# Kernel tuning notes

Hardware: AMD Instinct MI355X
Metric: run time of the kernel (lower is better)

The kernel has to match this reference:

```python
import jax, jax.numpy as jnp
import numpy as np

LN_EPS = 1e-5

def _layer_norm(x):
    m = jnp.mean(x, axis=-1, keepdims=True)
    v = jnp.mean(jnp.square(x - m), axis=-1, keepdims=True)
    return (x - m) / jnp.sqrt(v + LN_EPS)

def setup_inputs() -> dict:
    key = jax.random.key(0)
    ks = jax.random.split(key, 6)
    B, S, d_in, d_out = 8, 2048, 1024, 4096
    x = jax.random.normal(ks[0], (B, S, d_in), dtype=jnp.float32)
    # torch.randn % 1 -> values in [0, 1)
    weight_in = jax.random.uniform(ks[1], (d_out, d_in), dtype=jnp.float32)
    bias_in = jax.random.uniform(ks[2], (d_out,), dtype=jnp.float32)
    weight_out = jax.random.uniform(ks[3], (d_in, d_out), dtype=jnp.float32)
    bias_out = jax.random.uniform(ks[4], (d_in,), dtype=jnp.float32)
    lengths = jax.random.randint(ks[5], (B,), 1, S + 1, dtype=jnp.int64 if jax.config.read('jax_enable_x64') else jnp.int32)
    return {"x": x, "weight_in": weight_in, "bias_in": bias_in,
            "weight_out": weight_out, "bias_out": bias_out, "lengths": lengths}

def reference(x, weight_in, bias_in, weight_out, bias_out, lengths):
    # lengths is unused mathematically in the dense baseline (ragged kernels
    # only skip padded rows; valid-region math identical).
    for _ in range(10):
        x = jnp.einsum('bsd,od->bso', x, weight_in) + bias_in  # [B,S,d_out]
        x = _layer_norm(x)
        x = jnp.einsum('bso,do->bsd', x, weight_out) + bias_out  # [B,S,d_in]
        x = _layer_norm(x)
    return x
```

## Files before the change

kernel.cpp:

```cpp
#include <hip/hip_runtime.h>


typedef __attribute__((ext_vector_type(4))) float    f32x4;
typedef __attribute__((ext_vector_type(8))) _Float16 f16x8;
typedef __attribute__((ext_vector_type(4))) _Float16 f16x4;
typedef __attribute__((ext_vector_type(4))) uint     u32x4;

#define LN_EPS 1e-5f

__device__ __forceinline__ ushort f2h_bits(float f) {
    union { _Float16 h; ushort u; } c; c.h = (_Float16)f; return c.u;
}

typedef const __attribute__((address_space(1))) void* gas_ptr;
typedef __attribute__((address_space(3))) void* las_ptr;

__device__ __forceinline__ void gload_lds16(const void* g, void* l) {
    __builtin_amdgcn_global_load_lds((gas_ptr)g, (las_ptr)l, 16, 0, 0);
}

__device__ __forceinline__ f16x8 ldf(const _Float16* base, int byteoff) {
    return *reinterpret_cast<const f16x8*>(
        reinterpret_cast<const char*>(base) + byteoff);
}

__global__ __launch_bounds__(256) void conv_f32_f16(
        const float* __restrict__ in, _Float16* __restrict__ outp, int n4) {
    int i = blockIdx.x * 256 + threadIdx.x;
    if (i >= n4) return;
    float4 f = reinterpret_cast<const float4*>(in)[i];
    f16x4 r;
    r[0] = (_Float16)f.x; r[1] = (_Float16)f.y;
    r[2] = (_Float16)f.z; r[3] = (_Float16)f.w;
    *reinterpret_cast<f16x4*>(&outp[(size_t)i * 4]) = r;
}

template<int W>
__global__ __launch_bounds__(256)
void rowsum_rows(const _Float16* __restrict__ w, float* __restrict__ outp) {
    const int wid  = threadIdx.x >> 6;
    const int lane = threadIdx.x & 63;
    const size_t row = (size_t)blockIdx.x * 4 + wid;
    const _Float16* p = w + row * W;
    float s = 0.f;
    #pragma unroll
    for (int i = 0; i < W / 512; ++i) {
        f16x8 v = *reinterpret_cast<const f16x8*>(p + i * 512 + lane * 8);
        #pragma unroll
        for (int j = 0; j < 8; ++j) s += (float)v[j];
    }
    #pragma unroll
    for (int off = 32; off > 0; off >>= 1) s += __shfl_xor(s, off);
    if (lane == 0) outp[row] = s;
}

template<int M, int N, int K, bool FIRST>
__global__ __launch_bounds__(512)
void gemm256_ln(const _Float16* __restrict__ A, const _Float16* __restrict__ B,
                const float* __restrict__ bias, const float* __restrict__ wsum,
                const float2* __restrict__ pin, _Float16* __restrict__ C,
                float2* __restrict__ partials) {
    constexpr int NT   = K / 64;
    constexpr int NIT  = NT / 2;
    constexpr int NBX  = N / 256;
    constexpr int NWG  = (M / 256) * NBX;
    constexpr int NPIN = K / 256;

    __shared__ __attribute__((aligned(16))) _Float16 lds[2][2][2][8192];

    const int tid  = threadIdx.x;
    const int wid  = tid >> 6;
    const int lane = tid & 63;
    const int wr   = wid >> 2;
    const int wc   = wid & 3;

    int bn0, bm0;
    if constexpr (NBX == 16) {
        const int x = blockIdx.x & 7, j = blockIdx.x >> 3;
        bn0 = (x * 2 + (j & 1)) * 256;
        bm0 = (j >> 1) * 256;
    } else {
        int bid = (blockIdx.x & 7) * (NWG >> 3) + (blockIdx.x >> 3);
        bn0 = (bid % NBX) * 256;
        bm0 = (bid / NBX) * 256;
    }

    const int trow = tid >> 3;
    const int cg   = (tid & 7) ^ (trow & 7);
    const _Float16* Asrc = A + (size_t)(bm0 + trow) * K + cg * 8;
    const _Float16* Bsrc = B + (size_t)(bn0 + trow) * K + cg * 8;

    const int fr  = lane & 15;
    const int fq  = lane >> 4;
    const int s8  = lane & 7;
    const int cb0 = ((fq       ^ s8) << 4);
    const int cb1 = (((4 + fq) ^ s8) << 4);
    const int brb = (wc & 1) * 64;

    const _Float16* Ah[2] = { &lds[0][0][wr][0],      &lds[1][0][wr][0] };
    const _Float16* Bh[2] = { &lds[0][1][wc >> 1][0], &lds[1][1][wc >> 1][0] };

    f32x4 acc[8][4] = {};
    f16x8 aLo[4][2], aHi[4][2], bLo[2][2], bHi[2][2];

#define STAGE_A(buf, h, kk) do { \
    gload_lds16(Asrc + (size_t)((h)*128     ) * K + (kk), (void*)&lds[buf][0][h][       wid*512]); \
    gload_lds16(Asrc + (size_t)((h)*128 + 64) * K + (kk), (void*)&lds[buf][0][h][4096 + wid*512]); } while(0)
#define STAGE_B(buf, h, kk) do { \
    gload_lds16(Bsrc + (size_t)((h)*128     ) * K + (kk), (void*)&lds[buf][1][h][       wid*512]); \
    gload_lds16(Bsrc + (size_t)((h)*128 + 64) * K + (kk), (void*)&lds[buf][1][h][4096 + wid*512]); } while(0)

#define READ_ALO(b) do { _Pragma("unroll") for (int i = 0; i < 4; ++i) { \
    aLo[i][0] = ldf(Ah[b], (i*16+fr)*128 + cb0); \
    aLo[i][1] = ldf(Ah[b], (i*16+fr)*128 + cb1); } } while(0)
#define READ_AHI(b) do { _Pragma("unroll") for (int i = 0; i < 4; ++i) { \
    aHi[i][0] = ldf(Ah[b], ((i+4)*16+fr)*128 + cb0); \
    aHi[i][1] = ldf(Ah[b], ((i+4)*16+fr)*128 + cb1); } } while(0)
#define READ_BLO(b) do { _Pragma("unroll") for (int j = 0; j < 2; ++j) { \
    bLo[j][0] = ldf(Bh[b], (brb + j*16 + fr)*128 + cb0); \
    bLo[j][1] = ldf(Bh[b], (brb + j*16 + fr)*128 + cb1); } } while(0)
#define READ_BHI(b) do { _Pragma("unroll") for (int j = 0; j < 2; ++j) { \
    bHi[j][0] = ldf(Bh[b], (brb + (j+2)*16 + fr)*128 + cb0); \
    bHi[j][1] = ldf(Bh[b], (brb + (j+2)*16 + fr)*128 + cb1); } } while(0)

#define MFMA_BLK(AF, ioff, BF, joff) do { \
    _Pragma("unroll") for (int i = 0; i < 4; ++i) \
    _Pragma("unroll") for (int j = 0; j < 2; ++j) { \
        acc[i+ioff][j+joff] = __builtin_amdgcn_mfma_f32_16x16x32_f16(AF[i][0], BF[j][0], acc[i+ioff][j+joff], 0, 0, 0); \
        acc[i+ioff][j+joff] = __builtin_amdgcn_mfma_f32_16x16x32_f16(AF[i][1], BF[j][1], acc[i+ioff][j+joff], 0, 0, 0); } } while(0)

#define BARRIER() __builtin_amdgcn_s_barrier()
#define VMCNT4()  asm volatile("s_waitcnt vmcnt(4)" ::: "memory")
#define VMCNT0()  asm volatile("s_waitcnt vmcnt(0)" ::: "memory")

    STAGE_B(0, 0, 0);  STAGE_B(0, 1, 0);
    STAGE_A(0, 0, 0);  STAGE_A(0, 1, 0);
    STAGE_B(1, 0, 64); STAGE_B(1, 1, 64);

    float st_mean = 0.f, st_rstd = 1.f;
    if constexpr (!FIRST) {
        const int row  = tid >> 1;
        const int half = tid & 1;
        const float2* pr = pin + (size_t)(bm0 + row) * NPIN + half * (NPIN / 2);
        float s = 0.f, q = 0.f;
        #pragma unroll
        for (int k = 0; k < NPIN / 2; ++k) { s += pr[k].x; q += pr[k].y; }
        s += __shfl_xor(s, 1); q += __shfl_xor(q, 1);
        st_mean = s * (1.0f / K);
        const float var = fmaxf(q * (1.0f / K) - st_mean * st_mean, 0.f);
        st_rstd = rsqrtf(var + LN_EPS);
    }

    VMCNT4();
    BARRIER();

    float bcol[4], wcol[4];
    #pragma unroll
    for (int j = 0; j < 4; ++j) {
        const int c = bn0 + wc * 64 + j * 16 + fr;
        bcol[j] = bias[c]; wcol[j] = wsum[c];
    }

    for (int it = 0; it < NIT; ++it) {
        const int k1 = it * 128 + 64;
        const int k2 = (it * 128 + 128) & (K - 1);
        const int k3 = (it * 128 + 192) & (K - 1);
        const bool pf = (it < NIT - 1);

        READ_ALO(0); READ_BLO(0);
        STAGE_A(1, 0, k1);
        BARRIER();
        __builtin_amdgcn_s_setprio(1); MFMA_BLK(aLo, 0, bLo, 0); __builtin_amdgcn_s_setprio(0);
        BARRIER();
        READ_BHI(0);
        STAGE_A(1, 1, k1);
        BARRIER();
        __builtin_amdgcn_s_setprio(1); MFMA_BLK(aLo, 0, bHi, 2); __builtin_amdgcn_s_setprio(0);
        BARRIER();
        READ_AHI(0);
        if (pf) STAGE_B(0, 0, k2);
        BARRIER();
        __builtin_amdgcn_s_setprio(1); MFMA_BLK(aHi, 4, bLo, 0); __builtin_amdgcn_s_setprio(0);
        BARRIER();
        if (pf) STAGE_B(0, 1, k2);
        BARRIER();
        __builtin_amdgcn_s_setprio(1); MFMA_BLK(aHi, 4, bHi, 2); __builtin_amdgcn_s_setprio(0);
        if (pf) VMCNT4(); else VMCNT0();
        BARRIER();
        READ_ALO(1); READ_BLO(1);
        if (pf) STAGE_A(0, 0, k2);
        BARRIER();
        __builtin_amdgcn_s_setprio(1); MFMA_BLK(aLo, 0, bLo, 0); __builtin_amdgcn_s_setprio(0);
        BARRIER();
        READ_BHI(1);
        if (pf) STAGE_A(0, 1, k2);
        BARRIER();
        __builtin_amdgcn_s_setprio(1); MFMA_BLK(aLo, 0, bHi, 2); __builtin_amdgcn_s_setprio(0);
        BARRIER();
        READ_AHI(1);
        if (pf) STAGE_B(1, 0, k3);
        BARRIER();
        __builtin_amdgcn_s_setprio(1); MFMA_BLK(aHi, 4, bLo, 0); __builtin_amdgcn_s_setprio(0);
        BARRIER();
        if (pf) STAGE_B(1, 1, k3);
        BARRIER();
        __builtin_amdgcn_s_setprio(1); MFMA_BLK(aHi, 4, bHi, 2); __builtin_amdgcn_s_setprio(0);
        VMCNT4();
        BARRIER();
    }

    float2* sst = (float2*)&lds[0][0][0][0];
    if ((tid & 1) == 0) sst[tid >> 1] = make_float2(st_mean, st_rstd);
    __syncthreads();

    ushort* eps = (ushort*)&lds[1][0][0][0];
    #pragma unroll
    for (int pass = 0; pass < 4; ++pass) {
        if (wr == (pass >> 1)) {
            #pragma unroll
            for (int i2 = 0; i2 < 4; ++i2) {
                const int i = (pass & 1) * 4 + i2;
                #pragma unroll
                for (int q = 0; q < 4; ++q) {
                    const int rloc = wr * 128 + i * 16 + fq * 4 + q;
                    const int rl   = rloc - pass * 64;
                    const float2 st = sst[rloc];
                    const float rs = st.y, coef = st.y * st.x;
                    const int key = ((rl >> 2) & 3) << 4;
                    #pragma unroll
                    for (int j = 0; j < 4; ++j) {
                        const float v = rs * acc[i][j][q] - coef * wcol[j] + bcol[j];
                        const int c = wc * 64 + j * 16 + fr;
                        eps[rl * 256 + (c ^ key)] = f2h_bits(v);
                    }
                }
            }
        }
        BARRIER();
        {
            const int rl  = tid >> 3;
            const int a8  = tid & 7;
            const int r   = bm0 + pass * 64 + rl;
            const int key = ((rl >> 2) & 3) << 4;
            float s = 0.f, sq = 0.f;
            ushort* crow = (ushort*)(C + (size_t)r * N + bn0);
            #pragma unroll
            for (int k = 0; k < 4; ++k) {
                const int ch = 8 * k + a8;
                u32x4 d = *reinterpret_cast<const u32x4*>(&eps[rl * 256 + ch * 8]);
                const f16x8 v = *reinterpret_cast<const f16x8*>(&d);
                #pragma unroll
                for (int e = 0; e < 8; ++e) {
                    const float f = (float)v[e];
                    s += f; sq += f * f;
                }
                *reinterpret_cast<u32x4*>(&crow[(ch * 8) ^ key]) = d;
            }
            s  += __shfl_xor(s, 1);  sq += __shfl_xor(sq, 1);
            s  += __shfl_xor(s, 2);  sq += __shfl_xor(sq, 2);
            s  += __shfl_xor(s, 4);  sq += __shfl_xor(sq, 4);
            if (a8 == 0)
                partials[(size_t)r * NBX + (bn0 >> 8)] = make_float2(s, sq);
        }
        BARRIER();
    }
#undef STAGE_A
#undef STAGE_B
#undef READ_ALO
#undef READ_AHI
#undef READ_BLO
#undef READ_BHI
#undef MFMA_BLK
#undef BARRIER
#undef VMCNT4
#undef VMCNT0
}

__global__ __launch_bounds__(256)
void ln_final(const _Float16* __restrict__ a, const float2* __restrict__ part,
              float* __restrict__ outp) {
    const int wid  = threadIdx.x >> 6;
    const int lane = threadIdx.x & 63;
    const size_t row = (size_t)blockIdx.x * 4 + wid;

    float s = 0.f, q = 0.f;
    if (lane < 4) { const float2 p = part[row * 4 + lane]; s = p.x; q = p.y; }
    s += __shfl_xor(s, 1); q += __shfl_xor(q, 1);
    s += __shfl_xor(s, 2); q += __shfl_xor(q, 2);
    s = __shfl(s, 0); q = __shfl(q, 0);
    const float mean = s * (1.0f / 1024.f);
    const float var  = fmaxf(q * (1.0f / 1024.f) - mean * mean, 0.f);
    const float rstd = rsqrtf(var + LN_EPS);

    const _Float16* p = a + row * 1024;
    #pragma unroll
    for (int i = 0; i < 2; ++i) {
        f16x8 v = *reinterpret_cast<const f16x8*>(p + i * 512 + lane * 8);
        float* op = outp + row * 1024 + i * 512 + lane * 8;
        float4 o0, o1;
        o0.x = ((float)v[0] - mean) * rstd;
        o0.y = ((float)v[1] - mean) * rstd;
        o0.z = ((float)v[2] - mean) * rstd;
        o0.w = ((float)v[3] - mean) * rstd;
        o1.x = ((float)v[4] - mean) * rstd;
        o1.y = ((float)v[5] - mean) * rstd;
        o1.z = ((float)v[6] - mean) * rstd;
        o1.w = ((float)v[7] - mean) * rstd;
        reinterpret_cast<float4*>(op)[0] = o0;
        reinterpret_cast<float4*>(op)[1] = o1;
    }
}

extern "C" void kernel_launch(void* const* d_in, const int* in_sizes, int n_in,
                              void* d_out, int out_size, void* d_ws, size_t ws_size,
                              hipStream_t stream) {
    const float* x     = (const float*)d_in[0];
    const float* w_in  = (const float*)d_in[1];
    const float* b_in  = (const float*)d_in[2];
    const float* w_out = (const float*)d_in[3];
    const float* b_out = (const float*)d_in[4];

    constexpr int Mrows = 16384;
    constexpr int Din   = 1024;
    constexpr int Dout  = 4096;

    char* ws = (char*)d_ws;
    _Float16* wib = (_Float16*)ws; ws += (size_t)Dout * Din * 2;
    _Float16* wob = (_Float16*)ws; ws += (size_t)Din * Dout * 2;
    _Float16* a2b = (_Float16*)ws; ws += (size_t)Mrows * Din * 2;
    _Float16* a1b = (_Float16*)ws; ws += (size_t)Mrows * Dout * 2;
    float* winsum  = (float*)ws;   ws += Dout * 4;
    float* woutsum = (float*)ws;   ws += Din * 4;
    float2* p1  = (float2*)ws;     ws += (size_t)Mrows * 16 * 8;
    float2* p2  = (float2*)ws;

    const dim3 blk(256);

    conv_f32_f16<<<(Dout * Din / 4) / 256, blk, 0, stream>>>(w_in,  wib, Dout * Din / 4);
    conv_f32_f16<<<(Din * Dout / 4) / 256, blk, 0, stream>>>(w_out, wob, Din * Dout / 4);
    conv_f32_f16<<<(Mrows * Din / 4) / 256, blk, 0, stream>>>(x, a2b, Mrows * Din / 4);
    rowsum_rows<Din> <<<Dout / 4, blk, 0, stream>>>(wib, winsum);
    rowsum_rows<Dout><<<Din / 4,  blk, 0, stream>>>(wob, woutsum);

    for (int it = 0; it < 10; ++it) {
        if (it == 0)
            gemm256_ln<Mrows, Dout, Din, true>
                <<<(Mrows / 256) * (Dout / 256), dim3(512), 0, stream>>>(
                    a2b, wib, b_in, winsum, p2, a1b, p1);
        else
            gemm256_ln<Mrows, Dout, Din, false>
                <<<(Mrows / 256) * (Dout / 256), dim3(512), 0, stream>>>(
                    a2b, wib, b_in, winsum, p2, a1b, p1);
        gemm256_ln<Mrows, Din, Dout, false>
            <<<(Mrows / 256) * (Din / 256), dim3(512), 0, stream>>>(
                a1b, wob, b_out, woutsum, p1, a2b, p2);
    }
    ln_final<<<Mrows / 4, blk, 0, stream>>>(a2b, p2, (float*)d_out);
}
```

Baseline: 2.753 ms.

## Replace 256x256 GEMM tile with 128x256 tile and triple-buffered K32 pipeline

```diff
diff --git a/kernel.cpp b/kernel.cpp
--- a/kernel.cpp
+++ b/kernel.cpp
@@ -19,7 +19,7 @@
     __builtin_amdgcn_global_load_lds((gas_ptr)g, (las_ptr)l, 16, 0, 0);
 }
 
-__device__ __forceinline__ f16x8 ldf(const _Float16* base, int byteoff) {
+__device__ __forceinline__ f16x8 ldf(const ushort* base, int byteoff) {
     return *reinterpret_cast<const f16x8*>(
         reinterpret_cast<const char*>(base) + byteoff);
 }
@@ -55,18 +55,19 @@
 }
 
 template<int M, int N, int K, bool FIRST>
-__global__ __launch_bounds__(512)
-void gemm256_ln(const _Float16* __restrict__ A, const _Float16* __restrict__ B,
-                const float* __restrict__ bias, const float* __restrict__ wsum,
-                const float2* __restrict__ pin, _Float16* __restrict__ C,
-                float2* __restrict__ partials) {
-    constexpr int NT   = K / 64;
-    constexpr int NIT  = NT / 2;
+__global__ __launch_bounds__(512, 4)
+void gemm128_tri(const _Float16* __restrict__ A, const _Float16* __restrict__ B,
+                 const float* __restrict__ bias, const float* __restrict__ wsum,
+                 const float2* __restrict__ pin, _Float16* __restrict__ C,
+                 float2* __restrict__ partials) {
+    constexpr int NT   = K / 32;
     constexpr int NBX  = N / 256;
-    constexpr int NWG  = (M / 256) * NBX;
+    constexpr int NWG  = (M / 128) * NBX;
     constexpr int NPIN = K / 256;
-
-    __shared__ __attribute__((aligned(16))) _Float16 lds[2][2][2][8192];
+    constexpr int PE   = NPIN / 4;
+
+    __shared__ __attribute__((aligned(16))) ushort lds[3][12288];
+    __shared__ float2 sst[128];
 
     const int tid  = threadIdx.x;
     const int wid  = tid >> 6;
@@ -78,81 +79,79 @@
     if constexpr (NBX == 16) {
         const int x = blockIdx.x & 7, j = blockIdx.x >> 3;
         bn0 = (x * 2 + (j & 1)) * 256;
-        bm0 = (j >> 1) * 256;
+        bm0 = (j >> 1) * 128;
     } else {
         int bid = (blockIdx.x & 7) * (NWG >> 3) + (blockIdx.x >> 3);
         bn0 = (bid % NBX) * 256;
-        bm0 = (bid / NBX) * 256;
-    }
-
-    const int trow = tid >> 3;
-    const int cg   = (tid & 7) ^ (trow & 7);
+        bm0 = (bid / NBX) * 128;
+    }
+
+    const int trow = tid >> 2;
+    const int cg   = (tid & 3) ^ ((trow >> 1) & 3);
     const _Float16* Asrc = A + (size_t)(bm0 + trow) * K + cg * 8;
     const _Float16* Bsrc = B + (size_t)(bn0 + trow) * K + cg * 8;
 
-    const int fr  = lane & 15;
-    const int fq  = lane >> 4;
-    const int s8  = lane & 7;
-    const int cb0 = ((fq       ^ s8) << 4);
-    const int cb1 = (((4 + fq) ^ s8) << 4);
-    const int brb = (wc & 1) * 64;
-
-    const _Float16* Ah[2] = { &lds[0][0][wr][0],      &lds[1][0][wr][0] };
-    const _Float16* Bh[2] = { &lds[0][1][wc >> 1][0], &lds[1][1][wc >> 1][0] };
-
-    f32x4 acc[8][4] = {};
-    f16x8 aLo[4][2], aHi[4][2], bLo[2][2], bHi[2][2];
-
-#define STAGE_A(buf, h, kk) do { \
-    gload_lds16(Asrc + (size_t)((h)*128     ) * K + (kk), (void*)&lds[buf][0][h][       wid*512]); \
-    gload_lds16(Asrc + (size_t)((h)*128 + 64) * K + (kk), (void*)&lds[buf][0][h][4096 + wid*512]); } while(0)
-#define STAGE_B(buf, h, kk) do { \
-    gload_lds16(Bsrc + (size_t)((h)*128     ) * K + (kk), (void*)&lds[buf][1][h][       wid*512]); \
-    gload_lds16(Bsrc + (size_t)((h)*128 + 64) * K + (kk), (void*)&lds[buf][1][h][4096 + wid*512]); } while(0)
-
-#define READ_ALO(b) do { _Pragma("unroll") for (int i = 0; i < 4; ++i) { \
-    aLo[i][0] = ldf(Ah[b], (i*16+fr)*128 + cb0); \
-    aLo[i][1] = ldf(Ah[b], (i*16+fr)*128 + cb1); } } while(0)
-#define READ_AHI(b) do { _Pragma("unroll") for (int i = 0; i < 4; ++i) { \
-    aHi[i][0] = ldf(Ah[b], ((i+4)*16+fr)*128 + cb0); \
-    aHi[i][1] = ldf(Ah[b], ((i+4)*16+fr)*128 + cb1); } } while(0)
-#define READ_BLO(b) do { _Pragma("unroll") for (int j = 0; j < 2; ++j) { \
-    bLo[j][0] = ldf(Bh[b], (brb + j*16 + fr)*128 + cb0); \
-    bLo[j][1] = ldf(Bh[b], (brb + j*16 + fr)*128 + cb1); } } while(0)
-#define READ_BHI(b) do { _Pragma("unroll") for (int j = 0; j < 2; ++j) { \
-    bHi[j][0] = ldf(Bh[b], (brb + (j+2)*16 + fr)*128 + cb0); \
-    bHi[j][1] = ldf(Bh[b], (brb + (j+2)*16 + fr)*128 + cb1); } } while(0)
-
-#define MFMA_BLK(AF, ioff, BF, joff) do { \
-    _Pragma("unroll") for (int i = 0; i < 4; ++i) \
-    _Pragma("unroll") for (int j = 0; j < 2; ++j) { \
-        acc[i+ioff][j+joff] = __builtin_amdgcn_mfma_f32_16x16x32_f16(AF[i][0], BF[j][0], acc[i+ioff][j+joff], 0, 0, 0); \
-        acc[i+ioff][j+joff] = __builtin_amdgcn_mfma_f32_16x16x32_f16(AF[i][1], BF[j][1], acc[i+ioff][j+joff], 0, 0, 0); } } while(0)
+    const int fr = lane & 15;
+    const int fq = lane >> 4;
+    const int cb = ((fq ^ ((fr >> 1) & 3)) << 4);
+
+#define STAGE_T(buf, kk) do { \
+    gload_lds16(Asrc + (kk),                 (void*)&lds[buf][       wid * 512]); \
+    gload_lds16(Bsrc + (kk),                 (void*)&lds[buf][4096 + wid * 512]); \
+    gload_lds16(Bsrc + (size_t)128 * K + (kk), (void*)&lds[buf][8192 + wid * 512]); } while(0)
 
 #define BARRIER() __builtin_amdgcn_s_barrier()
-#define VMCNT4()  asm volatile("s_waitcnt vmcnt(4)" ::: "memory")
+#define VMCNT3()  asm volatile("s_waitcnt vmcnt(3)" ::: "memory")
 #define VMCNT0()  asm volatile("s_waitcnt vmcnt(0)" ::: "memory")
 
-    STAGE_B(0, 0, 0);  STAGE_B(0, 1, 0);
-    STAGE_A(0, 0, 0);  STAGE_A(0, 1, 0);
-    STAGE_B(1, 0, 64); STAGE_B(1, 1, 64);
+    STAGE_T(0, 0);
+    STAGE_T(1, 32);
 
     float st_mean = 0.f, st_rstd = 1.f;
     if constexpr (!FIRST) {
-        const int row  = tid >> 1;
-        const int half = tid & 1;
-        const float2* pr = pin + (size_t)(bm0 + row) * NPIN + half * (NPIN / 2);
+        const int row = tid >> 2, e = tid & 3;
+        const float2* pr = pin + (size_t)(bm0 + row) * NPIN + e * PE;
         float s = 0.f, q = 0.f;
         #pragma unroll
-        for (int k = 0; k < NPIN / 2; ++k) { s += pr[k].x; q += pr[k].y; }
+        for (int k = 0; k < PE; ++k) { s += pr[k].x; q += pr[k].y; }
         s += __shfl_xor(s, 1); q += __shfl_xor(q, 1);
+        s += __shfl_xor(s, 2); q += __shfl_xor(q, 2);
         st_mean = s * (1.0f / K);
         const float var = fmaxf(q * (1.0f / K) - st_mean * st_mean, 0.f);
         st_rstd = rsqrtf(var + LN_EPS);
     }
 
-    VMCNT4();
-    BARRIER();
+    f32x4 acc[4][4] = {};
+
+    for (int t = 0; t < NT; ++t) {
+        if (t < NT - 1) VMCNT3(); else VMCNT0();
+        BARRIER();
+        const int cur = t - (t / 3) * 3;
+        if (t + 2 < NT) {
+            const int nb = (t + 2) - ((t + 2) / 3) * 3;
+            STAGE_T(nb, (t + 2) * 32);
+        }
+        const ushort* Ab = &lds[cur][0];
+        const ushort* Bb = &lds[cur][4096];
+        f16x8 af[4], bf[4];
+        #pragma unroll
+        for (int i = 0; i < 4; ++i)
+            af[i] = ldf(Ab, (wr * 64 + i * 16 + fr) * 64 + cb);
+        #pragma unroll
+        for (int j = 0; j < 4; ++j)
+            bf[j] = ldf(Bb, (wc * 64 + j * 16 + fr) * 64 + cb);
+        __builtin_amdgcn_s_setprio(1);
+        #pragma unroll
+        for (int i = 0; i < 4; ++i)
+            #pragma unroll
+            for (int j = 0; j < 4; ++j)
+                acc[i][j] = __builtin_amdgcn_mfma_f32_16x16x32_f16(
+                    af[i], bf[j], acc[i][j], 0, 0, 0);
+        __builtin_amdgcn_s_setprio(0);
+    }
+
+    if ((tid & 3) == 0) sst[tid >> 2] = make_float2(st_mean, st_rstd);
+    __syncthreads();
 
     float bcol[4], wcol[4];
     #pragma unroll
@@ -161,118 +160,51 @@
         bcol[j] = bias[c]; wcol[j] = wsum[c];
     }
 
-    for (int it = 0; it < NIT; ++it) {
-        const int k1 = it * 128 + 64;
-        const int k2 = (it * 128 + 128) & (K - 1);
-        const int k3 = (it * 128 + 192) & (K - 1);
-        const bool pf = (it < NIT - 1);
-
-        READ_ALO(0); READ_BLO(0);
-        STAGE_A(1, 0, k1);
-        BARRIER();
-        __builtin_amdgcn_s_setprio(1); MFMA_BLK(aLo, 0, bLo, 0); __builtin_amdgcn_s_setprio(0);
-        BARRIER();
-        READ_BHI(0);
-        STAGE_A(1, 1, k1);
-        BARRIER();
-        __builtin_amdgcn_s_setprio(1); MFMA_BLK(aLo, 0, bHi, 2); __builtin_amdgcn_s_setprio(0);
-        BARRIER();
-        READ_AHI(0);
-        if (pf) STAGE_B(0, 0, k2);
-        BARRIER();
-        __builtin_amdgcn_s_setprio(1); MFMA_BLK(aHi, 4, bLo, 0); __builtin_amdgcn_s_setprio(0);
-        BARRIER();
-        if (pf) STAGE_B(0, 1, k2);
-        BARRIER();
-        __builtin_amdgcn_s_setprio(1); MFMA_BLK(aHi, 4, bHi, 2); __builtin_amdgcn_s_setprio(0);
-        if (pf) VMCNT4(); else VMCNT0();
-        BARRIER();
-        READ_ALO(1); READ_BLO(1);
-        if (pf) STAGE_A(0, 0, k2);
-        BARRIER();
-        __builtin_amdgcn_s_setprio(1); MFMA_BLK(aLo, 0, bLo, 0); __builtin_amdgcn_s_setprio(0);
-        BARRIER();
-        READ_BHI(1);
-        if (pf) STAGE_A(0, 1, k2);
-        BARRIER();
-        __builtin_amdgcn_s_setprio(1); MFMA_BLK(aLo, 0, bHi, 2); __builtin_amdgcn_s_setprio(0);
-        BARRIER();
-        READ_AHI(1);
-        if (pf) STAGE_B(1, 0, k3);
-        BARRIER();
-        __builtin_amdgcn_s_setprio(1); MFMA_BLK(aHi, 4, bLo, 0); __builtin_amdgcn_s_setprio(0);
-        BARRIER();
-        if (pf) STAGE_B(1, 1, k3);
-        BARRIER();
-        __builtin_amdgcn_s_setprio(1); MFMA_BLK(aHi, 4, bHi, 2); __builtin_amdgcn_s_setprio(0);
-        VMCNT4();
-        BARRIER();
-    }
-
-    float2* sst = (float2*)&lds[0][0][0][0];
-    if ((tid & 1) == 0) sst[tid >> 1] = make_float2(st_mean, st_rstd);
-    __syncthreads();
-
-    ushort* eps = (ushort*)&lds[1][0][0][0];
-    #pragma unroll
-    for (int pass = 0; pass < 4; ++pass) {
-        if (wr == (pass >> 1)) {
+    ushort* eps = &lds[0][0];
+    #pragma unroll
+    for (int i = 0; i < 4; ++i) {
+        #pragma unroll
+        for (int q = 0; q < 4; ++q) {
+            const int rloc = wr * 64 + i * 16 + fq * 4 + q;
+            const float2 st = sst[rloc];
+            const float rs = st.y, coef = st.y * st.x;
+            const int key = ((rloc >> 2) & 3) << 4;
             #pragma unroll
-            for (int i2 = 0; i2 < 4; ++i2) {
-                const int i = (pass & 1) * 4 + i2;
-                #pragma unroll
-                for (int q = 0; q < 4; ++q) {
-                    const int rloc = wr * 128 + i * 16 + fq * 4 + q;
-                    const int rl   = rloc - pass * 64;
-                    const float2 st = sst[rloc];
-                    const float rs = st.y, coef = st.y * st.x;
-                    const int key = ((rl >> 2) & 3) << 4;
-                    #pragma unroll
-                    for (int j = 0; j < 4; ++j) {
-                        const float v = rs * acc[i][j][q] - coef * wcol[j] + bcol[j];
-                        const int c = wc * 64 + j * 16 + fr;
-                        eps[rl * 256 + (c ^ key)] = f2h_bits(v);
-                    }
-                }
+            for (int j = 0; j < 4; ++j) {
+                const float v = rs * acc[i][j][q] - coef * wcol[j] + bcol[j];
+                const int c = wc * 64 + j * 16 + fr;
+                eps[rloc * 256 + (c ^ key)] = f2h_bits(v);
             }
         }
-        BARRIER();
-        {
-            const int rl  = tid >> 3;
-            const int a8  = tid & 7;
-            const int r   = bm0 + pass * 64 + rl;
-            const int key = ((rl >> 2) & 3) << 4;
-            float s = 0.f, sq = 0.f;
-            ushort* crow = (ushort*)(C + (size_t)r * N + bn0);
+    }
+    __syncthreads();
+
+    {
+        const int rl  = tid >> 2;
+        const int a4  = tid & 3;
+        const int key = ((rl >> 2) & 3) << 4;
+        float s = 0.f, sq = 0.f;
+        ushort* crow = (ushort*)(C + (size_t)(bm0 + rl) * N + bn0);
+        #pragma unroll
+        for (int k = 0; k < 8; ++k) {
+            const int ch = 4 * k + a4;
+            u32x4 d = *reinterpret_cast<const u32x4*>(&eps[rl * 256 + ch * 8]);
+            const f16x8 v = *reinterpret_cast<const f16x8*>(&d);
             #pragma unroll
-            for (int k = 0; k < 4; ++k) {
-                const int ch = 8 * k + a8;
-                u32x4 d = *reinterpret_cast<const u32x4*>(&eps[rl * 256 + ch * 8]);
-                const f16x8 v = *reinterpret_cast<const f16x8*>(&d);
-                #pragma unroll
-                for (int e = 0; e < 8; ++e) {
-                    const float f = (float)v[e];
-                    s += f; sq += f * f;
-                }
-                *reinterpret_cast<u32x4*>(&crow[(ch * 8) ^ key]) = d;
+            for (int e = 0; e < 8; ++e) {
+                const float f = (float)v[e];
+                s += f; sq += f * f;
             }
-            s  += __shfl_xor(s, 1);  sq += __shfl_xor(sq, 1);
-            s  += __shfl_xor(s, 2);  sq += __shfl_xor(sq, 2);
-            s  += __shfl_xor(s, 4);  sq += __shfl_xor(sq, 4);
-            if (a8 == 0)
-                partials[(size_t)r * NBX + (bn0 >> 8)] = make_float2(s, sq);
+            *reinterpret_cast<u32x4*>(&crow[(ch * 8) ^ key]) = d;
         }
-        BARRIER();
-    }
-#undef STAGE_A
-#undef STAGE_B
-#undef READ_ALO
-#undef READ_AHI
-#undef READ_BLO
-#undef READ_BHI
-#undef MFMA_BLK
+        s += __shfl_xor(s, 1); sq += __shfl_xor(sq, 1);
+        s += __shfl_xor(s, 2); sq += __shfl_xor(sq, 2);
+        if (a4 == 0)
+            partials[(size_t)(bm0 + rl) * NBX + (bn0 >> 8)] = make_float2(s, sq);
+    }
+#undef STAGE_T
 #undef BARRIER
-#undef VMCNT4
+#undef VMCNT3
 #undef VMCNT0
 }
 
@@ -344,15 +276,15 @@
 
     for (int it = 0; it < 10; ++it) {
         if (it == 0)
-            gemm256_ln<Mrows, Dout, Din, true>
-                <<<(Mrows / 256) * (Dout / 256), dim3(512), 0, stream>>>(
+            gemm128_tri<Mrows, Dout, Din, true>
+                <<<(Mrows / 128) * (Dout / 256), dim3(512), 0, stream>>>(
                     a2b, wib, b_in, winsum, p2, a1b, p1);
         else
-            gemm256_ln<Mrows, Dout, Din, false>
-                <<<(Mrows / 256) * (Dout / 256), dim3(512), 0, stream>>>(
+            gemm128_tri<Mrows, Dout, Din, false>
+                <<<(Mrows / 128) * (Dout / 256), dim3(512), 0, stream>>>(
                     a2b, wib, b_in, winsum, p2, a1b, p1);
-        gemm256_ln<Mrows, Din, Dout, false>
-            <<<(Mrows / 256) * (Din / 256), dim3(512), 0, stream>>>(
+        gemm128_tri<Mrows, Din, Dout, false>
+            <<<(Mrows / 128) * (Din / 256), dim3(512), 0, stream>>>(
                 a1b, wob, b_out, woutsum, p1, a2b, p2);
     }
     ln_final<<<Mrows / 4, blk, 0, stream>>>(a2b, p2, (float*)d_out);
```

Result: slower. 3.125 ms (+13.5%).

## Add 128x256-tile triple-buffered GEMM kernel for the first linear layer

Applied to the files above, without the earlier changes.

```diff
diff --git a/kernel.cpp b/kernel.cpp
--- a/kernel.cpp
+++ b/kernel.cpp
@@ -19,7 +19,11 @@
     __builtin_amdgcn_global_load_lds((gas_ptr)g, (las_ptr)l, 16, 0, 0);
 }
 
-__device__ __forceinline__ f16x8 ldf(const _Float16* base, int byteoff) {
+__device__ __forceinline__ f16x8 ldfus(const ushort* base, int byteoff) {
+    return *reinterpret_cast<const f16x8*>(
+        reinterpret_cast<const char*>(base) + byteoff);
+}
+__device__ __forceinline__ f16x8 ldfh(const _Float16* base, int byteoff) {
     return *reinterpret_cast<const f16x8*>(
         reinterpret_cast<const char*>(base) + byteoff);
 }
@@ -52,6 +56,159 @@
     #pragma unroll
     for (int off = 32; off > 0; off >>= 1) s += __shfl_xor(s, off);
     if (lane == 0) outp[row] = s;
+}
+
+template<int M, int N, int K, bool FIRST>
+__global__ __launch_bounds__(512, 4)
+void gemm128_tri(const _Float16* __restrict__ A, const _Float16* __restrict__ B,
+                 const float* __restrict__ bias, const float* __restrict__ wsum,
+                 const float2* __restrict__ pin, _Float16* __restrict__ C,
+                 float2* __restrict__ partials) {
+    constexpr int NT   = K / 32;
+    constexpr int NBX  = N / 256;
+    constexpr int NWG  = (M / 128) * NBX;
+    constexpr int NPIN = K / 256;
+    constexpr int PE   = NPIN / 4;
+
+    __shared__ __attribute__((aligned(16))) ushort lds[3][12288];
+    __shared__ float2 sst[128];
+
+    const int tid  = threadIdx.x;
+    const int wid  = tid >> 6;
+    const int lane = tid & 63;
+    const int wr   = wid >> 2;
+    const int wc   = wid & 3;
+
+    int bn0, bm0;
+    if constexpr (NBX == 16) {
+        const int x = blockIdx.x & 7, j = blockIdx.x >> 3;
+        bn0 = (x * 2 + (j & 1)) * 256;
+        bm0 = (j >> 1) * 128;
+    } else {
+        int bid = (blockIdx.x & 7) * (NWG >> 3) + (blockIdx.x >> 3);
+        bn0 = (bid % NBX) * 256;
+        bm0 = (bid / NBX) * 128;
+    }
+
+    const int trow = tid >> 2;
+    const int cg   = (tid & 3) ^ ((trow >> 1) & 3);
+    const _Float16* Asrc = A + (size_t)(bm0 + trow) * K + cg * 8;
+    const _Float16* Bsrc = B + (size_t)(bn0 + trow) * K + cg * 8;
+
+    const int fr = lane & 15;
+    const int fq = lane >> 4;
+    const int cb = ((fq ^ ((fr >> 1) & 3)) << 4);
+
+#define STAGE_T(buf, kk) do { \
+    gload_lds16(Asrc + (kk),                   (void*)&lds[buf][       wid * 512]); \
+    gload_lds16(Bsrc + (kk),                   (void*)&lds[buf][4096 + wid * 512]); \
+    gload_lds16(Bsrc + (size_t)128 * K + (kk), (void*)&lds[buf][8192 + wid * 512]); } while(0)
+#define BARRIER() __builtin_amdgcn_s_barrier()
+#define VMCNT3()  asm volatile("s_waitcnt vmcnt(3)" ::: "memory")
+#define VMCNT0()  asm volatile("s_waitcnt vmcnt(0)" ::: "memory")
+
+    STAGE_T(0, 0);
+    STAGE_T(1, 32);
+
+    float st_mean = 0.f, st_rstd = 1.f;
+    if constexpr (!FIRST) {
+        const int row = tid >> 2, e = tid & 3;
+        const float2* pr = pin + (size_t)(bm0 + row) * NPIN + e * PE;
+        float s = 0.f, q = 0.f;
+        #pragma unroll
+        for (int k = 0; k < PE; ++k) { s += pr[k].x; q += pr[k].y; }
+        s += __shfl_xor(s, 1); q += __shfl_xor(q, 1);
+        s += __shfl_xor(s, 2); q += __shfl_xor(q, 2);
+        st_mean = s * (1.0f / K);
+        const float var = fmaxf(q * (1.0f / K) - st_mean * st_mean, 0.f);
+        st_rstd = rsqrtf(var + LN_EPS);
+    }
+
+    f32x4 acc[4][4] = {};
+
+    for (int t = 0; t < NT; ++t) {
+        if (t < NT - 1) VMCNT3(); else VMCNT0();
+        BARRIER();
+        const int cur = t - (t / 3) * 3;
+        if (t + 2 < NT) {
+            const int nb = (t + 2) - ((t + 2) / 3) * 3;
+            STAGE_T(nb, (t + 2) * 32);
+        }
+        const ushort* Ab = &lds[cur][0];
+        const ushort* Bb = &lds[cur][4096];
+        f16x8 af[4], bf[4];
+        #pragma unroll
+        for (int i = 0; i < 4; ++i)
+            af[i] = ldfus(Ab, (wr * 64 + i * 16 + fr) * 64 + cb);
+        #pragma unroll
+        for (int j = 0; j < 4; ++j)
+            bf[j] = ldfus(Bb, (wc * 64 + j * 16 + fr) * 64 + cb);
+        __builtin_amdgcn_s_setprio(1);
+        #pragma unroll
+        for (int i = 0; i < 4; ++i)
+            #pragma unroll
+            for (int j = 0; j < 4; ++j)
+                acc[i][j] = __builtin_amdgcn_mfma_f32_16x16x32_f16(
+                    af[i], bf[j], acc[i][j], 0, 0, 0);
+        __builtin_amdgcn_s_setprio(0);
+    }
+
+    if ((tid & 3) == 0) sst[tid >> 2] = make_float2(st_mean, st_rstd);
+    __syncthreads();
+
+    float bcol[4], wcol[4];
+    #pragma unroll
+    for (int j = 0; j < 4; ++j) {
+        const int c = bn0 + wc * 64 + j * 16 + fr;
+        bcol[j] = bias[c]; wcol[j] = wsum[c];
+    }
+
+    ushort* eps = &lds[0][0];
+    #pragma unroll
+    for (int i = 0; i < 4; ++i) {
+        #pragma unroll
+        for (int q = 0; q < 4; ++q) {
+            const int rloc = wr * 64 + i * 16 + fq * 4 + q;
+            const float2 st = sst[rloc];
+            const float rs = st.y, coef = st.y * st.x;
+            const int key = ((rloc >> 2) & 3) << 4;
+            #pragma unroll
+            for (int j = 0; j < 4; ++j) {
+                const float v = rs * acc[i][j][q] - coef * wcol[j] + bcol[j];
+                const int c = wc * 64 + j * 16 + fr;
+                eps[rloc * 256 + (c ^ key)] = f2h_bits(v);
+            }
+        }
+    }
+    __syncthreads();
+
+    {
+        const int rl  = tid >> 2;
+        const int a4  = tid & 3;
+        const int key = ((rl >> 2) & 3) << 4;
+        float s = 0.f, sq = 0.f;
+        ushort* crow = (ushort*)(C + (size_t)(bm0 + rl) * N + bn0);
+        #pragma unroll
+        for (int k = 0; k < 8; ++k) {
+            const int ch = 4 * k + a4;
+            u32x4 d = *reinterpret_cast<const u32x4*>(&eps[rl * 256 + ch * 8]);
+            const f16x8 v = *reinterpret_cast<const f16x8*>(&d);
+            #pragma unroll
+            for (int e = 0; e < 8; ++e) {
+                const float f = (float)v[e];
+                s += f; sq += f * f;
+            }
+            *reinterpret_cast<u32x4*>(&crow[(ch * 8) ^ key]) = d;
+        }
+        s += __shfl_xor(s, 1); sq += __shfl_xor(sq, 1);
+        s += __shfl_xor(s, 2); sq += __shfl_xor(sq, 2);
+        if (a4 == 0)
+            partials[(size_t)(bm0 + rl) * NBX + (bn0 >> 8)] = make_float2(s, sq);
+    }
+#undef STAGE_T
+#undef BARRIER
+#undef VMCNT3
+#undef VMCNT0
 }
 
 template<int M, int N, int K, bool FIRST>
@@ -111,17 +268,17 @@
     gload_lds16(Bsrc + (size_t)((h)*128 + 64) * K + (kk), (void*)&lds[buf][1][h][4096 + wid*512]); } while(0)
 
 #define READ_ALO(b) do { _Pragma("unroll") for (int i = 0; i < 4; ++i) { \
-    aLo[i][0] = ldf(Ah[b], (i*16+fr)*128 + cb0); \
-    aLo[i][1] = ldf(Ah[b], (i*16+fr)*128 + cb1); } } while(0)
+    aLo[i][0] = ldfh(Ah[b], (i*16+fr)*128 + cb0); \
+    aLo[i][1] = ldfh(Ah[b], (i*16+fr)*128 + cb1); } } while(0)
 #define READ_AHI(b) do { _Pragma("unroll") for (int i = 0; i < 4; ++i) { \
-    aHi[i][0] = ldf(Ah[b], ((i+4)*16+fr)*128 + cb0); \
-    aHi[i][1] = ldf(Ah[b], ((i+4)*16+fr)*128 + cb1); } } while(0)
+    aHi[i][0] = ldfh(Ah[b], ((i+4)*16+fr)*128 + cb0); \
+    aHi[i][1] = ldfh(Ah[b], ((i+4)*16+fr)*128 + cb1); } } while(0)
 #define READ_BLO(b) do { _Pragma("unroll") for (int j = 0; j < 2; ++j) { \
-    bLo[j][0] = ldf(Bh[b], (brb + j*16 + fr)*128 + cb0); \
-    bLo[j][1] = ldf(Bh[b], (brb + j*16 + fr)*128 + cb1); } } while(0)
+    bLo[j][0] = ldfh(Bh[b], (brb + j*16 + fr)*128 + cb0); \
+    bLo[j][1] = ldfh(Bh[b], (brb + j*16 + fr)*128 + cb1); } } while(0)
 #define READ_BHI(b) do { _Pragma("unroll") for (int j = 0; j < 2; ++j) { \
-    bHi[j][0] = ldf(Bh[b], (brb + (j+2)*16 + fr)*128 + cb0); \
-    bHi[j][1] = ldf(Bh[b], (brb + (j+2)*16 + fr)*128 + cb1); } } while(0)
+    bHi[j][0] = ldfh(Bh[b], (brb + (j+2)*16 + fr)*128 + cb0); \
+    bHi[j][1] = ldfh(Bh[b], (brb + (j+2)*16 + fr)*128 + cb1); } } while(0)
 
 #define MFMA_BLK(AF, ioff, BF, joff) do { \
     _Pragma("unroll") for (int i = 0; i < 4; ++i) \
@@ -344,12 +501,12 @@
 
     for (int it = 0; it < 10; ++it) {
         if (it == 0)
-            gemm256_ln<Mrows, Dout, Din, true>
-                <<<(Mrows / 256) * (Dout / 256), dim3(512), 0, stream>>>(
+            gemm128_tri<Mrows, Dout, Din, true>
+                <<<(Mrows / 128) * (Dout / 256), dim3(512), 0, stream>>>(
                     a2b, wib, b_in, winsum, p2, a1b, p1);
         else
-            gemm256_ln<Mrows, Dout, Din, false>
-                <<<(Mrows / 256) * (Dout / 256), dim3(512), 0, stream>>>(
+            gemm128_tri<Mrows, Dout, Din, false>
+                <<<(Mrows / 128) * (Dout / 256), dim3(512), 0, stream>>>(
                     a2b, wib, b_in, winsum, p2, a1b, p1);
         gemm256_ln<Mrows, Din, Dout, false>
             <<<(Mrows / 256) * (Din / 256), dim3(512), 0, stream>>>(
```

After: 2.895 ms. 1.05x slower.
